# Kernel tuning notes

Measured on AMD Instinct MI355X. Metric: run time of the kernel, lower is better.

Reference implementation:

```python
import jax, jax.numpy as jnp
import numpy as np

N_MAPS = 6          # n: maps per class (5 kernels + 1 text)
N_CLASSES = 2       # len(text_classify)
RATIO = 3
LAMBDA = 0.7
EPS = 1e-4
NEG_INF = -1e30


def setup_inputs() -> dict:
    key = jax.random.key(0)
    k1, k2, k3 = jax.random.split(key, 3)
    B, C, H, W = 8, N_CLASSES * N_MAPS, 640, 640
    outputs = jax.random.normal(k1, (B, C, H, W), dtype=jnp.float32)
    labels = jax.random.uniform(k2, (B, C, H, W), dtype=jnp.float32)
    training_mask = jax.random.uniform(k3, (B, 1, H, W), dtype=jnp.float32)
    return {"outputs": outputs, "labels": labels, "training_mask": training_mask}


def _dice_loss(pred, target, mask):
    # pred/target: (B, HW) or (B, K, HW); mask broadcastable. sums over last axis.
    p = jax.nn.sigmoid(pred) * mask
    t = target * mask
    a = jnp.sum(p * t, axis=-1)
    b = jnp.sum(p * p, axis=-1) + EPS
    c = jnp.sum(t * t, axis=-1) + EPS
    return 1.0 - 2.0 * a / (b + c)


def _ohem_single(score, gt, tm):
    # score/gt/tm: (H, W). Returns float32 (H, W) selection mask.
    pos_num = jnp.sum((gt > 0.5) & (tm > 0.5))
    neg = gt <= 0.5
    neg_total = jnp.sum(neg)
    neg_num = jnp.minimum(pos_num * RATIO, neg_total)
    # descending sort of negative-position scores
    neg_sorted = -jnp.sort(-jnp.where(neg, score, NEG_INF).ravel())
    thr = neg_sorted[jnp.clip(neg_num - 1, 0, score.size - 1)]
    sel = ((score >= thr) | (gt > 0.5)) & (tm > 0.5)
    fallback = (pos_num == 0) | (neg_num == 0)
    return jnp.where(fallback, tm, sel.astype(jnp.float32))


def reference(outputs, labels, training_mask):
    B, C, H, W = outputs.shape
    tm = training_mask[:, 0]  # (B, H, W)
    text_losses, kernel_losses, class_losses = [], [], []
    for i in range(N_CLASSES):
        texts = outputs[:, (i + 1) * N_MAPS - 1]                 # (B, H, W)
        kernels = outputs[:, i * N_MAPS:(i + 1) * N_MAPS - 1]    # (B, K, H, W)
        gt_texts = labels[:, (i + 1) * N_MAPS - 1]
        gt_kernels = labels[:, i * N_MAPS:(i + 1) * N_MAPS - 1]
        # OHEM mask (detached in original via numpy round-trip)
        sel_text = jax.lax.stop_gradient(jax.vmap(_ohem_single)(texts, gt_texts, tm))
        loss_text = _dice_loss(texts.reshape(B, -1), gt_texts.reshape(B, -1),
                               sel_text.reshape(B, -1))  # (B,)
        # kernel mask: (sigmoid(texts) > 0.5) & (tm > 0.5), detached
        sel_k = jax.lax.stop_gradient(
            ((jax.nn.sigmoid(texts) > 0.5) & (tm > 0.5)).astype(jnp.float32))
        K = gt_kernels.shape[1]
        loss_kernels = _dice_loss(kernels.reshape(B, K, -1),
                                  gt_kernels.reshape(B, K, -1),
                                  sel_k.reshape(B, 1, -1))  # (B, K) per-kernel losses
        loss_kernels = jnp.mean(loss_kernels, axis=1)  # mean over kernels -> (B,)
        lt = jnp.mean(loss_text)      # reduction='mean'
        lk = jnp.mean(loss_kernels)
        loss = LAMBDA * lt + (1.0 - LAMBDA) * lk
        text_losses.append(lt)
        kernel_losses.append(lk)
        class_losses.append(loss)
    muti_class_loss_avg = jnp.mean(jnp.stack(class_losses))
    text_loss_avg = jnp.mean(jnp.stack(text_losses))
    kernel_loss_avg = jnp.mean(jnp.stack(kernel_losses))
    # stacked as (3,): [muti_class_loss_avg, text_loss_avg, kernel_loss_avg]
    return jnp.stack([muti_class_loss_avg, text_loss_avg, kernel_loss_avg])
```

## Files before the change

### kernel.cpp

```cpp
#include <hip/hip_runtime.h>

#define HW 409600
#define NCH 12

#define OFF_TACC   0
#define OFF_KACC   256
#define OFF_POS    2048
#define OFF_NEG    2112
#define OFF_MAXNK  2176
#define OFF_DONE   2240
#define OFF_FB     2304
#define OFF_NEGNUM 2368
#define OFF_THR    2432
#define OFF_META_END 2496
#define OFF_MASK   4096

__device__ __forceinline__ unsigned flipkey(float x){
  unsigned b = __float_as_uint(x);
  return (b & 0x80000000u) ? ~b : (b | 0x80000000u);
}
__device__ __forceinline__ float unflip(unsigned u){
  unsigned b = (u & 0x80000000u) ? (u ^ 0x80000000u) : ~u;
  return __uint_as_float(b);
}
__device__ __forceinline__ float sigmoidf(float x){
  return __fdividef(1.0f, 1.0f + __expf(-x));
}

__global__ __launch_bounds__(256) void k_main(
    const float* __restrict__ outputs, const float* __restrict__ labels,
    const float* __restrict__ tmask, unsigned char* __restrict__ maskb,
    unsigned* __restrict__ posA, unsigned* __restrict__ negA,
    unsigned* __restrict__ maxnkA, float* __restrict__ kacc)
{
  int img = blockIdx.x & 15;
  int blk = blockIdx.x >> 4;
  int ci = img >> 3, bi = img & 7;
  const size_t chb = (size_t)(bi*NCH + ci*6)*HW;
  const float* tp = outputs + chb + (size_t)5*HW;
  const float* gp = labels  + chb + (size_t)5*HW;
  const float* mp = tmask   + (size_t)bi*HW;
  int base = blk*2048 + (int)threadIdx.x*4;

  float4 tv0 = *(const float4*)(tp+base);
  float4 tv1 = *(const float4*)(tp+base+1024);
  float4 gv0 = *(const float4*)(gp+base);
  float4 gv1 = *(const float4*)(gp+base+1024);
  float4 mv0 = *(const float4*)(mp+base);
  float4 mv1 = *(const float4*)(mp+base+1024);
  float tt[8]={tv0.x,tv0.y,tv0.z,tv0.w, tv1.x,tv1.y,tv1.z,tv1.w};
  float gg[8]={gv0.x,gv0.y,gv0.z,gv0.w, gv1.x,gv1.y,gv1.z,gv1.w};
  float mm[8]={mv0.x,mv0.y,mv0.z,mv0.w, mv1.x,mv1.y,mv1.z,mv1.w};

  unsigned pos=0, neg=0, mn=0xFFFFFFFFu, selk=0;
  unsigned char mb[8];
  #pragma unroll
  for (int c=0;c<8;c++){
    bool isneg = (gg[c] <= 0.5f);
    bool tpos  = (mm[c] > 0.5f);
    pos += (unsigned)((!isneg) && tpos);
    neg += (unsigned)isneg;
    if ((tt[c] > 0.0f) && tpos) selk |= (1u<<c);
    mb[c] = (unsigned char)((isneg ? 0u : 1u) | (tpos ? 2u : 0u));
    if (isneg){ unsigned k = flipkey(tt[c]); mn = (k<mn)?k:mn; }
  }
  unsigned char* mw = maskb + (size_t)img*HW + base;
  *(uchar4*)(mw)      = make_uchar4(mb[0],mb[1],mb[2],mb[3]);
  *(uchar4*)(mw+1024) = make_uchar4(mb[4],mb[5],mb[6],mb[7]);

  const float* kp = outputs + chb;
  const float* lp = labels  + chb;
  float ka[5], kb_[5], kc[5];
  float4 a0 = *(const float4*)(kp+base);
  float4 a1 = *(const float4*)(kp+base+1024);
  float4 b0 = *(const float4*)(lp+base);
  float4 b1 = *(const float4*)(lp+base+1024);
  #pragma unroll
  for (int j=0;j<5;j++){
    float4 na0,na1,nb0,nb1;
    if (j<4){
      const float* kpn = kp + (size_t)(j+1)*HW;
      const float* lpn = lp + (size_t)(j+1)*HW;
      na0 = *(const float4*)(kpn+base);
      na1 = *(const float4*)(kpn+base+1024);
      nb0 = *(const float4*)(lpn+base);
      nb1 = *(const float4*)(lpn+base+1024);
    }
    float pa[8]={a0.x,a0.y,a0.z,a0.w, a1.x,a1.y,a1.z,a1.w};
    float ga[8]={b0.x,b0.y,b0.z,b0.w, b1.x,b1.y,b1.z,b1.w};
    float sa=0.f, sb=0.f, sc=0.f;
    #pragma unroll
    for (int c=0;c<8;c++){
      float m = ((selk>>c)&1u) ? 1.0f : 0.0f;
      float p = m * sigmoidf(pa[c]);
      float t = ga[c]*m;
      sa += p*t; sb += p*p; sc += t*t;
    }
    ka[j]=sa; kb_[j]=sb; kc[j]=sc;
    if (j<4){ a0=na0; a1=na1; b0=nb0; b1=nb1; }
  }

  #pragma unroll
  for (int o=32;o;o>>=1){
    #pragma unroll
    for (int j=0;j<5;j++){
      ka[j]  += __shfl_down(ka[j],o,64);
      kb_[j] += __shfl_down(kb_[j],o,64);
      kc[j]  += __shfl_down(kc[j],o,64);
    }
    pos += __shfl_down(pos,o,64);
    neg += __shfl_down(neg,o,64);
    unsigned om = __shfl_down(mn,o,64); mn = (om<mn)?om:mn;
  }
  __shared__ float sk[4][15];
  __shared__ unsigned spn[4][2], smn[4];
  int wv = threadIdx.x>>6, ln = threadIdx.x&63;
  if (ln==0){
    #pragma unroll
    for (int j=0;j<5;j++){ sk[wv][j]=ka[j]; sk[wv][5+j]=kb_[j]; sk[wv][10+j]=kc[j]; }
    spn[wv][0]=pos; spn[wv][1]=neg; smn[wv]=mn;
  }
  __syncthreads();
  if (threadIdx.x < 15){
    int j = threadIdx.x;
    float v = sk[0][j]+sk[1][j]+sk[2][j]+sk[3][j];
    int ch = j%5, comp = j/5;
    atomicAdd(&kacc[(img*5 + ch)*3 + comp], v);
  } else if (threadIdx.x == 32){
    atomicAdd(&posA[img], spn[0][0]+spn[1][0]+spn[2][0]+spn[3][0]);
    atomicAdd(&negA[img], spn[0][1]+spn[1][1]+spn[2][1]+spn[3][1]);
    unsigned m01 = (smn[0]<smn[1])?smn[0]:smn[1];
    unsigned m23 = (smn[2]<smn[3])?smn[2]:smn[3];
    unsigned m = (m01<m23)?m01:m23;
    atomicMax(&maxnkA[img], ~m);
  }
}

__global__ void k_decide(
    const unsigned* __restrict__ posA, const unsigned* __restrict__ negA,
    const unsigned* __restrict__ maxnkA, unsigned* __restrict__ doneA,
    unsigned* __restrict__ fbA, unsigned* __restrict__ negnumA,
    float* __restrict__ thrA)
{
  int img = threadIdx.x;
  if (img >= 16) return;
  unsigned pos = posA[img], negt = negA[img];
  unsigned p3 = pos*3u;
  unsigned negnum = (p3 < negt) ? p3 : negt;
  if (pos==0u || negnum==0u){
    doneA[img]=1u; fbA[img]=1u; negnumA[img]=1u; thrA[img]=0.0f;
  } else if (negnum == negt){
    doneA[img]=1u; fbA[img]=0u; negnumA[img]=negnum;
    thrA[img] = unflip(~maxnkA[img]);
  } else {
    doneA[img]=0u; fbA[img]=0u; negnumA[img]=negnum; thrA[img]=0.0f;
  }
}

__global__ __launch_bounds__(1024) void k_fallback(
    const float* __restrict__ outputs, const unsigned char* __restrict__ maskb,
    const unsigned* __restrict__ doneA, const unsigned* __restrict__ negnumA,
    float* __restrict__ thrA)
{
  int img = blockIdx.x;
  if (doneA[img]) return;
  int ci=img>>3, bi=img&7;
  const float* tp = outputs + (size_t)(bi*NCH+ci*6+5)*HW;
  const unsigned char* mk = maskb + (size_t)img*HW;
  __shared__ unsigned lh[2048];
  __shared__ unsigned sel_s, krem_s;
  unsigned k = negnumA[img];
  unsigned prefix = 0;
  for (int round=0; round<3; round++){
    for (int j=threadIdx.x; j<2048; j+=1024) lh[j]=0u;
    __syncthreads();
    for (int it=0; it<100; it++){
      int px = it*4096 + (int)threadIdx.x*4;
      float4 tv = *(const float4*)(tp+px);
      uchar4 mq = *(const uchar4*)(mk+px);
      float tt[4]={tv.x,tv.y,tv.z,tv.w};
      unsigned char ma[4]={mq.x,mq.y,mq.z,mq.w};
      #pragma unroll
      for (int c=0;c<4;c++){
        if (!(ma[c]&1)){
          unsigned key = flipkey(tt[c]);
          unsigned bin; bool ok;
          if (round==0){ bin = key>>21; ok = true; }
          else if (round==1){ ok = ((key>>21)==prefix); bin = (key>>10)&0x7FFu; }
          else { ok = ((key>>10)==prefix); bin = key & 0x3FFu; }
          if (ok) atomicAdd(&lh[bin], 1u);
        }
      }
    }
    __syncthreads();
    if (threadIdx.x==0){
      int nb = (round==2) ? 1024 : 2048;
      unsigned cum=0, sel=0, kr=1;
      for (int x=nb-1; x>=0; x--){
        cum += lh[x];
        if (cum >= k){ sel=(unsigned)x; kr = k - (cum - lh[x]); break; }
      }
      sel_s=sel; krem_s=kr;
    }
    __syncthreads();
    k = krem_s;
    prefix = (round==0) ? sel_s : ((prefix<<11) | sel_s);
    if (round==2 && threadIdx.x==0) thrA[img] = unflip((prefix<<10) >> 10 == prefix ? prefix : prefix);
    __syncthreads();
  }
  if (threadIdx.x==0){
    unsigned p22 = prefix >> 11;
    unsigned sel3 = prefix & 0x7FFu;
    thrA[img] = unflip((p22<<10) | sel3);
  }
}

__global__ __launch_bounds__(256) void k_text(
    const float* __restrict__ outputs, const float* __restrict__ labels,
    const float* __restrict__ tmask, const unsigned char* __restrict__ maskb,
    const unsigned* __restrict__ fbA, const float* __restrict__ thrA,
    float* __restrict__ tacc)
{
  int img = blockIdx.x & 15;
  int blk = blockIdx.x >> 4;
  int ci=img>>3, bi=img&7;
  const float* tp = outputs + (size_t)(bi*NCH+ci*6+5)*HW;
  const float* gp = labels  + (size_t)(bi*NCH+ci*6+5)*HW;
  const unsigned char* mk = maskb + (size_t)img*HW;
  int base = blk*2048 + (int)threadIdx.x*4;
  bool fb = (fbA[img] != 0u);
  float thr = thrA[img];

  float4 tv0 = *(const float4*)(tp+base);
  float4 tv1 = *(const float4*)(tp+base+1024);
  float4 gv0 = *(const float4*)(gp+base);
  float4 gv1 = *(const float4*)(gp+base+1024);
  uchar4 m0 = *(const uchar4*)(mk+base);
  uchar4 m1 = *(const uchar4*)(mk+base+1024);
  float tt[8]={tv0.x,tv0.y,tv0.z,tv0.w, tv1.x,tv1.y,tv1.z,tv1.w};
  float gg[8]={gv0.x,gv0.y,gv0.z,gv0.w, gv1.x,gv1.y,gv1.z,gv1.w};
  unsigned char ma[8]={m0.x,m0.y,m0.z,m0.w, m1.x,m1.y,m1.z,m1.w};
  float ta[8]={0,0,0,0,0,0,0,0};
  if (fb){
    const float* mp = tmask + (size_t)bi*HW;
    float4 x0 = *(const float4*)(mp+base);
    float4 x1 = *(const float4*)(mp+base+1024);
    ta[0]=x0.x;ta[1]=x0.y;ta[2]=x0.z;ta[3]=x0.w;
    ta[4]=x1.x;ta[5]=x1.y;ta[6]=x1.z;ta[7]=x1.w;
  }
  float sa=0.f, sb=0.f, sc=0.f;
  #pragma unroll
  for (int c=0;c<8;c++){
    float m;
    if (fb) m = ta[c];
    else    m = (((tt[c] >= thr) || (ma[c]&1)) && (ma[c]&2)) ? 1.0f : 0.0f;
    float p = m * sigmoidf(tt[c]);
    float t = gg[c]*m;
    sa += p*t; sb += p*p; sc += t*t;
  }
  #pragma unroll
  for (int o=32;o;o>>=1){
    sa += __shfl_down(sa,o,64); sb += __shfl_down(sb,o,64); sc += __shfl_down(sc,o,64);
  }
  __shared__ float ra[4], rb[4], rc[4];
  int wv=threadIdx.x>>6, ln=threadIdx.x&63;
  if (ln==0){ ra[wv]=sa; rb[wv]=sb; rc[wv]=sc; }
  __syncthreads();
  if (threadIdx.x==0){
    atomicAdd(&tacc[img*3+0], ra[0]+ra[1]+ra[2]+ra[3]);
    atomicAdd(&tacc[img*3+1], rb[0]+rb[1]+rb[2]+rb[3]);
    atomicAdd(&tacc[img*3+2], rc[0]+rc[1]+rc[2]+rc[3]);
  }
}

__global__ void k_final(const float* __restrict__ tacc, const float* __restrict__ kacc,
                        float* __restrict__ out)
{
  if (blockIdx.x==0 && threadIdx.x==0){
    const float EPSF = 1e-4f;
    float ltA[2], lkA[2];
    for (int i=0;i<2;i++){
      float lt=0.f;
      for (int b=0;b<8;b++){
        int img=i*8+b;
        float a=tacc[img*3], p2=tacc[img*3+1]+EPSF, t2=tacc[img*3+2]+EPSF;
        lt += 1.f - 2.f*a/(p2+t2);
      }
      lt *= 0.125f;
      float lk=0.f;
      for (int b=0;b<8;b++) for (int k=0;k<5;k++){
        int idx=((i*8+b)*5+k)*3;
        float a=kacc[idx], p2=kacc[idx+1]+EPSF, t2=kacc[idx+2]+EPSF;
        lk += 1.f - 2.f*a/(p2+t2);
      }
      lk /= 40.f;
      ltA[i]=lt; lkA[i]=lk;
    }
    float l0 = 0.7f*ltA[0] + 0.3f*lkA[0];
    float l1 = 0.7f*ltA[1] + 0.3f*lkA[1];
    out[0]=0.5f*(l0+l1);
    out[1]=0.5f*(ltA[0]+ltA[1]);
    out[2]=0.5f*(lkA[0]+lkA[1]);
  }
}

extern "C" void kernel_launch(void* const* d_in, const int* in_sizes, int n_in,
                              void* d_out, int out_size, void* d_ws, size_t ws_size,
                              hipStream_t stream)
{
  const float* outputs = (const float*)d_in[0];
  const float* labels  = (const float*)d_in[1];
  const float* tmask   = (const float*)d_in[2];
  float* out = (float*)d_out;
  char* ws = (char*)d_ws;
  float* tacc      = (float*)(ws + OFF_TACC);
  float* kacc      = (float*)(ws + OFF_KACC);
  unsigned* posA   = (unsigned*)(ws + OFF_POS);
  unsigned* negA   = (unsigned*)(ws + OFF_NEG);
  unsigned* maxnkA = (unsigned*)(ws + OFF_MAXNK);
  unsigned* doneA  = (unsigned*)(ws + OFF_DONE);
  unsigned* fbA    = (unsigned*)(ws + OFF_FB);
  unsigned* negnumA= (unsigned*)(ws + OFF_NEGNUM);
  float* thrA      = (float*)(ws + OFF_THR);
  unsigned char* maskb = (unsigned char*)(ws + OFF_MASK);

  hipMemsetAsync(ws, 0, OFF_META_END, stream);
  k_main    <<<3200,256,0,stream>>>(outputs, labels, tmask, maskb, posA, negA, maxnkA, kacc);
  k_decide  <<<1,64,0,stream>>>(posA, negA, maxnkA, doneA, fbA, negnumA, thrA);
  k_fallback<<<16,1024,0,stream>>>(outputs, maskb, doneA, negnumA, thrA);
  k_text    <<<3200,256,0,stream>>>(outputs, labels, tmask, maskb, fbA, thrA, tacc);
  k_final   <<<1,64,0,stream>>>(tacc, kacc, out);
}
```

Baseline: 410.6 us.

## Fold decide kernel into fallback and text kernels, restructure main loads

Removes the separate single-block decide kernel by recomputing the positive/negative counts and threshold decision inside k_fallback and k_text, saving one launch and its serialization. k_main is restructured to process two 4-pixel chunks per thread, issuing all kernel-channel loads up front, with a launch-bounds occupancy hint. The mask byte encoding changes (negative bit moved to bit 2), and k_text now reads gt directly for the positive check. The extra loads raise register pressure, which the occupancy hint may force into spills.

Result: no change. 410.7 us (+0.0%).

```diff
diff --git a/kernel.cpp b/kernel.cpp
--- a/kernel.cpp
+++ b/kernel.cpp
@@ -5,14 +5,11 @@
 
 #define OFF_TACC   0
 #define OFF_KACC   256
-#define OFF_POS    2048
-#define OFF_NEG    2112
-#define OFF_MAXNK  2176
-#define OFF_DONE   2240
-#define OFF_FB     2304
-#define OFF_NEGNUM 2368
-#define OFF_THR    2432
-#define OFF_META_END 2496
+#define OFF_POS    1280
+#define OFF_NEG    1344
+#define OFF_MAXNK  1408
+#define OFF_THR    1472
+#define OFF_META_END 1536
 #define OFF_MASK   4096
 
 __device__ __forceinline__ unsigned flipkey(float x){
@@ -27,7 +24,7 @@
   return __fdividef(1.0f, 1.0f + __expf(-x));
 }
 
-__global__ __launch_bounds__(256) void k_main(
+__global__ __launch_bounds__(256,4) void k_main(
     const float* __restrict__ outputs, const float* __restrict__ labels,
     const float* __restrict__ tmask, unsigned char* __restrict__ maskb,
     unsigned* __restrict__ posA, unsigned* __restrict__ negA,
@@ -40,64 +37,53 @@
   const float* tp = outputs + chb + (size_t)5*HW;
   const float* gp = labels  + chb + (size_t)5*HW;
   const float* mp = tmask   + (size_t)bi*HW;
-  int base = blk*2048 + (int)threadIdx.x*4;
-
-  float4 tv0 = *(const float4*)(tp+base);
-  float4 tv1 = *(const float4*)(tp+base+1024);
-  float4 gv0 = *(const float4*)(gp+base);
-  float4 gv1 = *(const float4*)(gp+base+1024);
-  float4 mv0 = *(const float4*)(mp+base);
-  float4 mv1 = *(const float4*)(mp+base+1024);
-  float tt[8]={tv0.x,tv0.y,tv0.z,tv0.w, tv1.x,tv1.y,tv1.z,tv1.w};
-  float gg[8]={gv0.x,gv0.y,gv0.z,gv0.w, gv1.x,gv1.y,gv1.z,gv1.w};
-  float mm[8]={mv0.x,mv0.y,mv0.z,mv0.w, mv1.x,mv1.y,mv1.z,mv1.w};
-
-  unsigned pos=0, neg=0, mn=0xFFFFFFFFu, selk=0;
-  unsigned char mb[8];
-  #pragma unroll
-  for (int c=0;c<8;c++){
-    bool isneg = (gg[c] <= 0.5f);
-    bool tpos  = (mm[c] > 0.5f);
-    pos += (unsigned)((!isneg) && tpos);
-    neg += (unsigned)isneg;
-    if ((tt[c] > 0.0f) && tpos) selk |= (1u<<c);
-    mb[c] = (unsigned char)((isneg ? 0u : 1u) | (tpos ? 2u : 0u));
-    if (isneg){ unsigned k = flipkey(tt[c]); mn = (k<mn)?k:mn; }
-  }
-  unsigned char* mw = maskb + (size_t)img*HW + base;
-  *(uchar4*)(mw)      = make_uchar4(mb[0],mb[1],mb[2],mb[3]);
-  *(uchar4*)(mw+1024) = make_uchar4(mb[4],mb[5],mb[6],mb[7]);
-
   const float* kp = outputs + chb;
   const float* lp = labels  + chb;
-  float ka[5], kb_[5], kc[5];
-  float4 a0 = *(const float4*)(kp+base);
-  float4 a1 = *(const float4*)(kp+base+1024);
-  float4 b0 = *(const float4*)(lp+base);
-  float4 b1 = *(const float4*)(lp+base+1024);
+
+  float ka[5]={0,0,0,0,0}, kb_[5]={0,0,0,0,0}, kc[5]={0,0,0,0,0};
+  unsigned pos=0, neg=0, mn=0xFFFFFFFFu;
+
   #pragma unroll
-  for (int j=0;j<5;j++){
-    float4 na0,na1,nb0,nb1;
-    if (j<4){
-      const float* kpn = kp + (size_t)(j+1)*HW;
-      const float* lpn = lp + (size_t)(j+1)*HW;
-      na0 = *(const float4*)(kpn+base);
-      na1 = *(const float4*)(kpn+base+1024);
-      nb0 = *(const float4*)(lpn+base);
-      nb1 = *(const float4*)(lpn+base+1024);
-    }
-    float pa[8]={a0.x,a0.y,a0.z,a0.w, a1.x,a1.y,a1.z,a1.w};
-    float ga[8]={b0.x,b0.y,b0.z,b0.w, b1.x,b1.y,b1.z,b1.w};
-    float sa=0.f, sb=0.f, sc=0.f;
-    #pragma unroll
-    for (int c=0;c<8;c++){
-      float m = ((selk>>c)&1u) ? 1.0f : 0.0f;
-      float p = m * sigmoidf(pa[c]);
-      float t = ga[c]*m;
-      sa += p*t; sb += p*p; sc += t*t;
-    }
-    ka[j]=sa; kb_[j]=sb; kc[j]=sc;
-    if (j<4){ a0=na0; a1=na1; b0=nb0; b1=nb1; }
+  for (int k=0;k<2;k++){
+    int px = blk*2048 + k*1024 + (int)threadIdx.x*4;
+    float4 tv = *(const float4*)(tp+px);
+    float4 gv = *(const float4*)(gp+px);
+    float4 mv = *(const float4*)(mp+px);
+    float4 av[5], bv[5];
+    #pragma unroll
+    for (int j=0;j<5;j++){
+      av[j] = *(const float4*)(kp + (size_t)j*HW + px);
+      bv[j] = *(const float4*)(lp + (size_t)j*HW + px);
+    }
+    float tt[4]={tv.x,tv.y,tv.z,tv.w};
+    float gg[4]={gv.x,gv.y,gv.z,gv.w};
+    float mm[4]={mv.x,mv.y,mv.z,mv.w};
+    float msel[4];
+    unsigned char mb[4];
+    #pragma unroll
+    for (int c=0;c<4;c++){
+      bool isneg = (gg[c] <= 0.5f);
+      bool tpos  = (mm[c] > 0.5f);
+      bool selk  = (tt[c] > 0.0f) && tpos;
+      pos += (unsigned)((!isneg) && tpos);
+      neg += (unsigned)isneg;
+      msel[c] = selk ? 1.0f : 0.0f;
+      mb[c] = (unsigned char)((selk?1u:0u) | (tpos?2u:0u) | (isneg?4u:0u));
+      if (isneg){ unsigned kk = flipkey(tt[c]); mn = (kk<mn)?kk:mn; }
+    }
+    *(uchar4*)(maskb + (size_t)img*HW + px) = make_uchar4(mb[0],mb[1],mb[2],mb[3]);
+    #pragma unroll
+    for (int j=0;j<5;j++){
+      float pa[4]={av[j].x,av[j].y,av[j].z,av[j].w};
+      float ga[4]={bv[j].x,bv[j].y,bv[j].z,bv[j].w};
+      #pragma unroll
+      for (int c=0;c<4;c++){
+        float m = msel[c];
+        float p = m * sigmoidf(pa[c]);
+        float t = ga[c]*m;
+        ka[j] += p*t; kb_[j] += p*p; kc[j] += t*t;
+      }
+    }
   }
 
   #pragma unroll
@@ -126,50 +112,31 @@
     float v = sk[0][j]+sk[1][j]+sk[2][j]+sk[3][j];
     int ch = j%5, comp = j/5;
     atomicAdd(&kacc[(img*5 + ch)*3 + comp], v);
-  } else if (threadIdx.x == 32){
+  } else if (threadIdx.x == 64){
     atomicAdd(&posA[img], spn[0][0]+spn[1][0]+spn[2][0]+spn[3][0]);
     atomicAdd(&negA[img], spn[0][1]+spn[1][1]+spn[2][1]+spn[3][1]);
     unsigned m01 = (smn[0]<smn[1])?smn[0]:smn[1];
     unsigned m23 = (smn[2]<smn[3])?smn[2]:smn[3];
-    unsigned m = (m01<m23)?m01:m23;
-    atomicMax(&maxnkA[img], ~m);
-  }
-}
-
-__global__ void k_decide(
+    atomicMax(&maxnkA[img], ~((m01<m23)?m01:m23));
+  }
+}
+
+__global__ __launch_bounds__(1024) void k_fallback(
+    const float* __restrict__ outputs, const unsigned char* __restrict__ maskb,
     const unsigned* __restrict__ posA, const unsigned* __restrict__ negA,
-    const unsigned* __restrict__ maxnkA, unsigned* __restrict__ doneA,
-    unsigned* __restrict__ fbA, unsigned* __restrict__ negnumA,
     float* __restrict__ thrA)
 {
-  int img = threadIdx.x;
-  if (img >= 16) return;
+  int img = blockIdx.x;
   unsigned pos = posA[img], negt = negA[img];
   unsigned p3 = pos*3u;
   unsigned negnum = (p3 < negt) ? p3 : negt;
-  if (pos==0u || negnum==0u){
-    doneA[img]=1u; fbA[img]=1u; negnumA[img]=1u; thrA[img]=0.0f;
-  } else if (negnum == negt){
-    doneA[img]=1u; fbA[img]=0u; negnumA[img]=negnum;
-    thrA[img] = unflip(~maxnkA[img]);
-  } else {
-    doneA[img]=0u; fbA[img]=0u; negnumA[img]=negnum; thrA[img]=0.0f;
-  }
-}
-
-__global__ __launch_bounds__(1024) void k_fallback(
-    const float* __restrict__ outputs, const unsigned char* __restrict__ maskb,
-    const unsigned* __restrict__ doneA, const unsigned* __restrict__ negnumA,
-    float* __restrict__ thrA)
-{
-  int img = blockIdx.x;
-  if (doneA[img]) return;
+  if (pos==0u || negnum==0u || negnum==negt) return;
   int ci=img>>3, bi=img&7;
   const float* tp = outputs + (size_t)(bi*NCH+ci*6+5)*HW;
   const unsigned char* mk = maskb + (size_t)img*HW;
   __shared__ unsigned lh[2048];
   __shared__ unsigned sel_s, krem_s;
-  unsigned k = negnumA[img];
+  unsigned k = negnum;
   unsigned prefix = 0;
   for (int round=0; round<3; round++){
     for (int j=threadIdx.x; j<2048; j+=1024) lh[j]=0u;
@@ -182,7 +149,7 @@
       unsigned char ma[4]={mq.x,mq.y,mq.z,mq.w};
       #pragma unroll
       for (int c=0;c<4;c++){
-        if (!(ma[c]&1)){
+        if (ma[c]&4){
           unsigned key = flipkey(tt[c]);
           unsigned bin; bool ok;
           if (round==0){ bin = key>>21; ok = true; }
@@ -205,12 +172,11 @@
     __syncthreads();
     k = krem_s;
     prefix = (round==0) ? sel_s : ((prefix<<11) | sel_s);
-    if (round==2 && threadIdx.x==0) thrA[img] = unflip((prefix<<10) >> 10 == prefix ? prefix : prefix);
     __syncthreads();
   }
   if (threadIdx.x==0){
-    unsigned p22 = prefix >> 11;
-    unsigned sel3 = prefix & 0x7FFu;
+    unsigned p22  = prefix >> 11;
+    unsigned sel3 = prefix & 0x3FFu;
     thrA[img] = unflip((p22<<10) | sel3);
   }
 }
@@ -218,7 +184,8 @@
 __global__ __launch_bounds__(256) void k_text(
     const float* __restrict__ outputs, const float* __restrict__ labels,
     const float* __restrict__ tmask, const unsigned char* __restrict__ maskb,
-    const unsigned* __restrict__ fbA, const float* __restrict__ thrA,
+    const unsigned* __restrict__ posA, const unsigned* __restrict__ negA,
+    const unsigned* __restrict__ maxnkA, const float* __restrict__ thrA,
     float* __restrict__ tacc)
 {
   int img = blockIdx.x & 15;
@@ -228,8 +195,15 @@
   const float* gp = labels  + (size_t)(bi*NCH+ci*6+5)*HW;
   const unsigned char* mk = maskb + (size_t)img*HW;
   int base = blk*2048 + (int)threadIdx.x*4;
-  bool fb = (fbA[img] != 0u);
-  float thr = thrA[img];
+
+  unsigned pos = posA[img], negt = negA[img];
+  unsigned p3 = pos*3u;
+  unsigned negnum = (p3 < negt) ? p3 : negt;
+  bool fb = (pos==0u || negnum==0u);
+  float thr;
+  if (fb)                    thr = 0.0f;
+  else if (negnum == negt)   thr = unflip(~maxnkA[img]);
+  else                       thr = thrA[img];
 
   float4 tv0 = *(const float4*)(tp+base);
   float4 tv1 = *(const float4*)(tp+base+1024);
@@ -253,7 +227,7 @@
   for (int c=0;c<8;c++){
     float m;
     if (fb) m = ta[c];
-    else    m = (((tt[c] >= thr) || (ma[c]&1)) && (ma[c]&2)) ? 1.0f : 0.0f;
+    else    m = (((tt[c] >= thr) || (gg[c] > 0.5f)) && (ma[c]&2)) ? 1.0f : 0.0f;
     float p = m * sigmoidf(tt[c]);
     float t = gg[c]*m;
     sa += p*t; sb += p*p; sc += t*t;
@@ -318,16 +292,12 @@
   unsigned* posA   = (unsigned*)(ws + OFF_POS);
   unsigned* negA   = (unsigned*)(ws + OFF_NEG);
   unsigned* maxnkA = (unsigned*)(ws + OFF_MAXNK);
-  unsigned* doneA  = (unsigned*)(ws + OFF_DONE);
-  unsigned* fbA    = (unsigned*)(ws + OFF_FB);
-  unsigned* negnumA= (unsigned*)(ws + OFF_NEGNUM);
   float* thrA      = (float*)(ws + OFF_THR);
   unsigned char* maskb = (unsigned char*)(ws + OFF_MASK);
 
   hipMemsetAsync(ws, 0, OFF_META_END, stream);
   k_main    <<<3200,256,0,stream>>>(outputs, labels, tmask, maskb, posA, negA, maxnkA, kacc);
-  k_decide  <<<1,64,0,stream>>>(posA, negA, maxnkA, doneA, fbA, negnumA, thrA);
-  k_fallback<<<16,1024,0,stream>>>(outputs, maskb, doneA, negnumA, thrA);
-  k_text    <<<3200,256,0,stream>>>(outputs, labels, tmask, maskb, fbA, thrA, tacc);
+  k_fallback<<<16,1024,0,stream>>>(outputs, maskb, posA, negA, thrA);
+  k_text    <<<3200,256,0,stream>>>(outputs, labels, tmask, maskb, posA, negA, maxnkA, thrA, tacc);
   k_final   <<<1,64,0,stream>>>(tacc, kacc, out);
 }
```
